# Kernel tuning notes

Hardware: AMD Instinct MI355X
Metric: run time of the kernel (lower is better)

Reference implementation:

```python
import jax, jax.numpy as jnp
import numpy as np

N_NODES = 100000


def _sage_layer(x, src, dst, Wl, Wr, b):
    # mean-aggregate source features at destination nodes
    msgs = x[src]                                                # [E, d_in]
    agg = jax.ops.segment_sum(msgs, dst, num_segments=N_NODES)  # [N, d_in]
    cnt = jax.ops.segment_sum(jnp.ones((src.shape[0], 1), x.dtype), dst,
                              num_segments=N_NODES)             # [N, 1]
    mean = agg / jnp.maximum(cnt, 1.0)
    # PyG SAGEConv: lin_l(aggr) + lin_r(x); lin_l carries the bias
    return mean @ Wl.T + x @ Wr.T + b


def setup_inputs() -> dict:
    key = jax.random.key(0)
    ks = jax.random.split(key, 9)
    d_in, d_h, d_out, E = 128, 128, 64, 1600000
    s = 1.0 / np.sqrt(d_in)
    inp = {
        "x": jax.random.normal(ks[0], (N_NODES, d_in), jnp.float32),
        "Wl0": jax.random.normal(ks[1], (d_h, d_in), jnp.float32) * s,
        "Wr0": jax.random.normal(ks[2], (d_h, d_in), jnp.float32) * s,
        "b0": jnp.zeros((d_h,), jnp.float32),
        "Wl1": jax.random.normal(ks[3], (d_h, d_h), jnp.float32) * s,
        "Wr1": jax.random.normal(ks[4], (d_h, d_h), jnp.float32) * s,
        "b1": jnp.zeros((d_h,), jnp.float32),
        "Wl2": jax.random.normal(ks[5], (d_out, d_h), jnp.float32) * s,
        "Wr2": jax.random.normal(ks[6], (d_out, d_h), jnp.float32) * s,
        "b2": jnp.zeros((d_out,), jnp.float32),
        "edge_index": jax.random.randint(ks[7], (2, E), 0, N_NODES, jnp.int64),
    }
    return inp


def reference(x, Wl0, Wr0, b0, Wl1, Wr1, b1, Wl2, Wr2, b2, edge_index):
    src, dst = edge_index[0], edge_index[1]
    h = jax.nn.relu(_sage_layer(x, src, dst, Wl0, Wr0, b0))  # dropout = identity (eval)
    h = jax.nn.relu(_sage_layer(h, src, dst, Wl1, Wr1, b1))
    return _sage_layer(h, src, dst, Wl2, Wr2, b2)
```

## Files before the change

### kernel.cpp

```cpp
#include <hip/hip_runtime.h>

#define D 128
typedef unsigned short u16;
typedef unsigned int u32;
typedef __attribute__((ext_vector_type(8))) short short8;
typedef __attribute__((ext_vector_type(16))) float float16;

__device__ __forceinline__ u16 f2bf(float f) {
    u32 u = __builtin_bit_cast(u32, f);
    u += 0x7FFFu + ((u >> 16) & 1u);
    return (u16)(u >> 16);
}
__device__ __forceinline__ float bf2f(u16 b) {
    return __builtin_bit_cast(float, ((u32)b) << 16);
}
__device__ __forceinline__ short8 zero8() {
    short8 z;
    #pragma unroll
    for (int i = 0; i < 8; ++i) z[i] = 0;
    return z;
}


__global__ __launch_bounds__(256) void hist_kernel(const int* __restrict__ dst,
        int* __restrict__ cnt, int* __restrict__ rank, int E) {
    int e = blockIdx.x * 256 + threadIdx.x;
    if (e < E) rank[e] = atomicAdd(&cnt[dst[e]], 1);
}

__global__ __launch_bounds__(256) void scan1_kernel(const int* __restrict__ cnt,
        int* __restrict__ rowptr, int* __restrict__ blksum, int N) {
    __shared__ int sdata[256];
    const int base = blockIdx.x * 1024 + threadIdx.x * 4;
    int v0 = 0, v1 = 0, v2 = 0, v3 = 0;
    if (base + 3 < N) {
        int4 q = *reinterpret_cast<const int4*>(cnt + base);
        v0 = q.x; v1 = q.y; v2 = q.z; v3 = q.w;
    } else {
        if (base + 0 < N) v0 = cnt[base + 0];
        if (base + 1 < N) v1 = cnt[base + 1];
        if (base + 2 < N) v2 = cnt[base + 2];
    }
    const int t = v0 + v1 + v2 + v3;
    int val = t;
    sdata[threadIdx.x] = val;
    __syncthreads();
    for (int off = 1; off < 256; off <<= 1) {
        int other = (threadIdx.x >= off) ? sdata[threadIdx.x - off] : 0;
        __syncthreads();
        val += other;
        sdata[threadIdx.x] = val;
        __syncthreads();
    }
    const int excl = val - t;
    if (base + 0 < N) rowptr[base + 0] = excl;
    if (base + 1 < N) rowptr[base + 1] = excl + v0;
    if (base + 2 < N) rowptr[base + 2] = excl + v0 + v1;
    if (base + 3 < N) rowptr[base + 3] = excl + v0 + v1 + v2;
    if (threadIdx.x == 255) blksum[blockIdx.x] = val;
}

__global__ __launch_bounds__(256) void scan2_kernel(int* __restrict__ blksum, int nb) {
    __shared__ int s[256];
    const int t = threadIdx.x;
    const int v = (t < nb) ? blksum[t] : 0;
    int val = v;
    s[t] = val;
    __syncthreads();
    for (int off = 1; off < 256; off <<= 1) {
        int o = (t >= off) ? s[t - off] : 0;
        __syncthreads();
        val += o;
        s[t] = val;
        __syncthreads();
    }
    if (t < nb) blksum[t] = val - v;
    if (t == 255) blksum[nb] = val;
}

__global__ __launch_bounds__(256) void scan3_kernel(int* __restrict__ rowptr,
        const int* __restrict__ blksum, int N) {
    const int base = blockIdx.x * 1024 + threadIdx.x * 4;
    const int off = blksum[blockIdx.x];
    #pragma unroll
    for (int k = 0; k < 4; ++k)
        if (base + k < N) rowptr[base + k] += off;
    if (base == 0 && blockIdx.x == 0) rowptr[N] = blksum[gridDim.x];
}

__global__ __launch_bounds__(256) void invdeg_kernel(const int* __restrict__ rowptr,
        float* __restrict__ invd, int N) {
    int i = blockIdx.x * 256 + threadIdx.x;
    if (i < N) {
        int deg = rowptr[i + 1] - rowptr[i];
        invd[i] = 1.0f / (float)(deg > 1 ? deg : 1);
    }
}

__global__ __launch_bounds__(256) void fill_kernel(const int* __restrict__ src,
        const int* __restrict__ dst, const int* __restrict__ rowptr,
        const int* __restrict__ rank, int* __restrict__ colidx, int E) {
    int e = blockIdx.x * 256 + threadIdx.x;
    if (e < E) {
        int d = dst[e];
        colidx[rowptr[d] + rank[e]] = src[e];
    }
}

__global__ __launch_bounds__(256) void tobf16_kernel(const float* __restrict__ in,
        u16* __restrict__ outb, int n8) {
    int i = blockIdx.x * 256 + threadIdx.x;
    if (i >= n8) return;
    float4 a = *reinterpret_cast<const float4*>(in + (size_t)i * 8);
    float4 b = *reinterpret_cast<const float4*>(in + (size_t)i * 8 + 4);
    short8 r;
    r[0] = (short)f2bf(a.x); r[1] = (short)f2bf(a.y);
    r[2] = (short)f2bf(a.z); r[3] = (short)f2bf(a.w);
    r[4] = (short)f2bf(b.x); r[5] = (short)f2bf(b.y);
    r[6] = (short)f2bf(b.z); r[7] = (short)f2bf(b.w);
    *reinterpret_cast<short8*>(outb + (size_t)i * 8) = r;
}

__global__ __launch_bounds__(256) void gather_kernel(const u16* __restrict__ xin,
        const int* __restrict__ rowptr, const int* __restrict__ colidx,
        const float* __restrict__ invd, u16* __restrict__ outA, int N) {
    const int node = blockIdx.x * 4 + (threadIdx.x >> 6);
    if (node >= N) return;
    const int lane = threadIdx.x & 63;
    const int g = lane >> 4;
    const int r = lane & 15;
    const int beg = rowptr[node];
    const int nb = rowptr[node + 1] - beg;

    float a0 = 0.f, a1 = 0.f, a2 = 0.f, a3 = 0.f;
    float a4 = 0.f, a5 = 0.f, a6 = 0.f, a7 = 0.f;

    for (int base = 0; base < nb; base += 8) {
        const bool p0 = (base + g) < nb;
        const bool p1 = (base + 4 + g) < nb;
        uint4 v0 = make_uint4(0, 0, 0, 0), v1 = v0;
        if (p0) {
            int s0 = colidx[beg + base + g];
            v0 = *reinterpret_cast<const uint4*>(xin + (size_t)s0 * D + r * 8);
        }
        if (p1) {
            int s1 = colidx[beg + base + 4 + g];
            v1 = *reinterpret_cast<const uint4*>(xin + (size_t)s1 * D + r * 8);
        }
        a0 += bf2f((u16)v0.x) + bf2f((u16)v1.x);
        a1 += bf2f((u16)(v0.x >> 16)) + bf2f((u16)(v1.x >> 16));
        a2 += bf2f((u16)v0.y) + bf2f((u16)v1.y);
        a3 += bf2f((u16)(v0.y >> 16)) + bf2f((u16)(v1.y >> 16));
        a4 += bf2f((u16)v0.z) + bf2f((u16)v1.z);
        a5 += bf2f((u16)(v0.z >> 16)) + bf2f((u16)(v1.z >> 16));
        a6 += bf2f((u16)v0.w) + bf2f((u16)v1.w);
        a7 += bf2f((u16)(v0.w >> 16)) + bf2f((u16)(v1.w >> 16));
    }

    #pragma unroll
    for (int m = 16; m <= 32; m <<= 1) {
        a0 += __shfl_xor(a0, m, 64); a1 += __shfl_xor(a1, m, 64);
        a2 += __shfl_xor(a2, m, 64); a3 += __shfl_xor(a3, m, 64);
        a4 += __shfl_xor(a4, m, 64); a5 += __shfl_xor(a5, m, 64);
        a6 += __shfl_xor(a6, m, 64); a7 += __shfl_xor(a7, m, 64);
    }

    if (g == 0) {
        const float ic = invd[node];
        uint4 o;
        o.x = (u32)f2bf(a0 * ic) | ((u32)f2bf(a1 * ic) << 16);
        o.y = (u32)f2bf(a2 * ic) | ((u32)f2bf(a3 * ic) << 16);
        o.z = (u32)f2bf(a4 * ic) | ((u32)f2bf(a5 * ic) << 16);
        o.w = (u32)f2bf(a6 * ic) | ((u32)f2bf(a7 * ic) << 16);
        *reinterpret_cast<uint4*>(outA + (size_t)node * D + r * 8) = o;
    }
}

__global__ __launch_bounds__(256) void gather64_kernel(const u16* __restrict__ yin,
        const int* __restrict__ rowptr, const int* __restrict__ colidx,
        const float* __restrict__ invd, u16* __restrict__ outM, int N) {
    const int node = blockIdx.x * 4 + (threadIdx.x >> 6);
    if (node >= N) return;
    const int lane = threadIdx.x & 63;
    const int g = lane >> 4;
    const int r = lane & 15;
    const int beg = rowptr[node];
    const int nb = rowptr[node + 1] - beg;

    float a0 = 0.f, a1 = 0.f, a2 = 0.f, a3 = 0.f;

    for (int base = 0; base < nb; base += 8) {
        const bool p0 = (base + g) < nb;
        const bool p1 = (base + 4 + g) < nb;
        uint2 v0 = make_uint2(0, 0), v1 = v0;
        if (p0) {
            int s0 = colidx[beg + base + g];
            v0 = *reinterpret_cast<const uint2*>(yin + (size_t)s0 * 64 + r * 4);
        }
        if (p1) {
            int s1 = colidx[beg + base + 4 + g];
            v1 = *reinterpret_cast<const uint2*>(yin + (size_t)s1 * 64 + r * 4);
        }
        a0 += bf2f((u16)v0.x) + bf2f((u16)v1.x);
        a1 += bf2f((u16)(v0.x >> 16)) + bf2f((u16)(v1.x >> 16));
        a2 += bf2f((u16)v0.y) + bf2f((u16)v1.y);
        a3 += bf2f((u16)(v0.y >> 16)) + bf2f((u16)(v1.y >> 16));
    }

    #pragma unroll
    for (int m = 16; m <= 32; m <<= 1) {
        a0 += __shfl_xor(a0, m, 64); a1 += __shfl_xor(a1, m, 64);
        a2 += __shfl_xor(a2, m, 64); a3 += __shfl_xor(a3, m, 64);
    }

    if (g == 0) {
        const float ic = invd[node];
        uint2 o;
        o.x = (u32)f2bf(a0 * ic) | ((u32)f2bf(a1 * ic) << 16);
        o.y = (u32)f2bf(a2 * ic) | ((u32)f2bf(a3 * ic) << 16);
        *reinterpret_cast<uint2*>(outM + (size_t)node * 64 + r * 4) = o;
    }
}

template<int DOUT, bool RELU, bool BF16OUT>
__global__ __launch_bounds__(256) void sage_gemm(
    const u16* __restrict__ Abf, const u16* __restrict__ Xbf,
    const float* __restrict__ Wl, const float* __restrict__ Wr,
    const float* __restrict__ bias, float* __restrict__ outf,
    u16* __restrict__ outb, int N, int nchunks)
{
    constexpr int BM = 256;
    constexpr int NKB = 4;
    constexpr int WR = (DOUT == 128) ? 2 : 4;
    constexpr int WC = 4 / WR;
    constexpr int WTM = BM / WR;
    constexpr int WTN = DOUT / WC;
    constexpr int MR = WTM / 32;
    constexpr int NC = WTN / 32;
    constexpr int LDA = 72;
    constexpr int LDW = 264;

    __shared__ u16 sW[DOUT][LDW];
    __shared__ u16 sA[2][BM][LDA];

    const int tid = threadIdx.x;
    const int lane = tid & 63;
    const int w = tid >> 6;
    const int wr = w % WR;
    const int wc = w / WR;

    for (int i = tid; i < DOUT * 64; i += 256) {
        const int c = i >> 6, q = i & 63;
        const float* sp = (q < 32) ? (Wl + (size_t)c * 128 + q * 4)
                                   : (Wr + (size_t)c * 128 + (q - 32) * 4);
        float4 wv = *reinterpret_cast<const float4*>(sp);
        u32* dp = reinterpret_cast<u32*>(&sW[c][q * 4]);
        dp[0] = (u32)f2bf(wv.x) | ((u32)f2bf(wv.y) << 16);
        dp[1] = (u32)f2bf(wv.z) | ((u32)f2bf(wv.w) << 16);
    }

    short8 rg[2][4];

    auto STAGE = [&](int kb, int m0) {
        const u16* srcb = (kb < 2) ? Abf : Xbf;
        const int koff = (kb & 1) * 64;
        #pragma unroll
        for (int p = 0; p < 2; ++p) {
            const int r = (tid >> 1) + p * 128;
            const int row = m0 + r;
            const u16* sp = srcb + (size_t)row * D + koff + (tid & 1) * 32;
            if (row < N) {
                #pragma unroll
                for (int uu = 0; uu < 4; ++uu)
                    rg[p][uu] = *reinterpret_cast<const short8*>(sp + uu * 8);
            } else {
                #pragma unroll
                for (int uu = 0; uu < 4; ++uu) rg[p][uu] = zero8();
            }
        }
    };
    auto WLDS = [&](int buf) {
        #pragma unroll
        for (int p = 0; p < 2; ++p) {
            const int r = (tid >> 1) + p * 128;
            u16* dp = &sA[buf][r][(tid & 1) * 32];
            #pragma unroll
            for (int uu = 0; uu < 4; ++uu)
                *reinterpret_cast<short8*>(dp + uu * 8) = rg[p][uu];
        }
    };

    for (int chunk = blockIdx.x; chunk < nchunks; chunk += gridDim.x) {
        const int m0 = chunk * BM;
        STAGE(0, m0);
        __syncthreads();
        WLDS(0);

        float16 acc[MR][NC];
        #pragma unroll
        for (int mi = 0; mi < MR; ++mi)
            #pragma unroll
            for (int ni = 0; ni < NC; ++ni)
                #pragma unroll
                for (int e = 0; e < 16; ++e) acc[mi][ni][e] = 0.f;

        #pragma unroll
        for (int kb = 0; kb < NKB; ++kb) {
            if (kb + 1 < NKB) STAGE(kb + 1, m0);
            __syncthreads();
            #pragma unroll
            for (int ks = 0; ks < 4; ++ks) {
                short8 af[MR], bfv[NC];
                #pragma unroll
                for (int mi = 0; mi < MR; ++mi)
                    af[mi] = *reinterpret_cast<const short8*>(
                        &sA[kb & 1][wr * WTM + mi * 32 + (lane & 31)]
                           [ks * 16 + (lane >> 5) * 8]);
                #pragma unroll
                for (int ni = 0; ni < NC; ++ni)
                    bfv[ni] = *reinterpret_cast<const short8*>(
                        &sW[wc * WTN + ni * 32 + (lane & 31)]
                           [kb * 64 + ks * 16 + (lane >> 5) * 8]);
                #pragma unroll
                for (int mi = 0; mi < MR; ++mi)
                    #pragma unroll
                    for (int ni = 0; ni < NC; ++ni)
                        acc[mi][ni] = __builtin_amdgcn_mfma_f32_32x32x16_bf16(
                            af[mi], bfv[ni], acc[mi][ni], 0, 0, 0);
            }
            if (kb + 1 < NKB) WLDS((kb + 1) & 1);
        }

        #pragma unroll
        for (int ni = 0; ni < NC; ++ni) {
            const int col = wc * WTN + ni * 32 + (lane & 31);
            const float bv = bias[col];
            #pragma unroll
            for (int mi = 0; mi < MR; ++mi) {
                #pragma unroll
                for (int e = 0; e < 16; ++e) {
                    const int row = wr * WTM + mi * 32 + 4 * (lane >> 5)
                                    + (e & 3) + 8 * (e >> 2);
                    const int grow = m0 + row;
                    if (grow < N) {
                        float v = acc[mi][ni][e] + bv;
                        if (RELU) v = fmaxf(v, 0.f);
                        if (BF16OUT) outb[(size_t)grow * DOUT + col] = f2bf(v);
                        else         outf[(size_t)grow * DOUT + col] = v;
                    }
                }
            }
        }
    }
}

template<bool ADDMEAN, bool BF16OUT, bool BIAS>
__global__ __launch_bounds__(256) void lin_gemm(
    const u16* __restrict__ In, const float* __restrict__ W,
    const float* __restrict__ bias, const u16* __restrict__ mean2,
    float* __restrict__ outf, u16* __restrict__ outb, int N, int nchunks)
{
    constexpr int DOUT = 64;
    constexpr int BM = 256;
    constexpr int NKB = 2;
    constexpr int WTM = 64;
    constexpr int MR = 2, NC = 2;
    constexpr int LDA = 72;
    constexpr int LDW = 136;

    __shared__ u16 sW[DOUT][LDW];
    __shared__ u16 sA[2][BM][LDA];

    const int tid = threadIdx.x;
    const int lane = tid & 63;
    const int wr = tid >> 6;

    for (int i = tid; i < DOUT * 32; i += 256) {
        const int c = i >> 5, q = i & 31;
        float4 wv = *reinterpret_cast<const float4*>(W + (size_t)c * 128 + q * 4);
        u32* dp = reinterpret_cast<u32*>(&sW[c][q * 4]);
        dp[0] = (u32)f2bf(wv.x) | ((u32)f2bf(wv.y) << 16);
        dp[1] = (u32)f2bf(wv.z) | ((u32)f2bf(wv.w) << 16);
    }

    short8 rg[2][4];

    auto STAGE = [&](int kb, int m0) {
        const int koff = kb * 64;
        #pragma unroll
        for (int p = 0; p < 2; ++p) {
            const int r = (tid >> 1) + p * 128;
            const int row = m0 + r;
            const u16* sp = In + (size_t)row * D + koff + (tid & 1) * 32;
            if (row < N) {
                #pragma unroll
                for (int uu = 0; uu < 4; ++uu)
                    rg[p][uu] = *reinterpret_cast<const short8*>(sp + uu * 8);
            } else {
                #pragma unroll
                for (int uu = 0; uu < 4; ++uu) rg[p][uu] = zero8();
            }
        }
    };
    auto WLDS = [&](int buf) {
        #pragma unroll
        for (int p = 0; p < 2; ++p) {
            const int r = (tid >> 1) + p * 128;
            u16* dp = &sA[buf][r][(tid & 1) * 32];
            #pragma unroll
            for (int uu = 0; uu < 4; ++uu)
                *reinterpret_cast<short8*>(dp + uu * 8) = rg[p][uu];
        }
    };

    for (int chunk = blockIdx.x; chunk < nchunks; chunk += gridDim.x) {
        const int m0 = chunk * BM;
        STAGE(0, m0);
        __syncthreads();
        WLDS(0);

        float16 acc[MR][NC];
        #pragma unroll
        for (int mi = 0; mi < MR; ++mi)
            #pragma unroll
            for (int ni = 0; ni < NC; ++ni)
                #pragma unroll
                for (int e = 0; e < 16; ++e) acc[mi][ni][e] = 0.f;

        #pragma unroll
        for (int kb = 0; kb < NKB; ++kb) {
            if (kb + 1 < NKB) STAGE(kb + 1, m0);
            __syncthreads();
            #pragma unroll
            for (int ks = 0; ks < 4; ++ks) {
                short8 af[MR], bfv[NC];
                #pragma unroll
                for (int mi = 0; mi < MR; ++mi)
                    af[mi] = *reinterpret_cast<const short8*>(
                        &sA[kb & 1][wr * WTM + mi * 32 + (lane & 31)]
                           [ks * 16 + (lane >> 5) * 8]);
                #pragma unroll
                for (int ni = 0; ni < NC; ++ni)
                    bfv[ni] = *reinterpret_cast<const short8*>(
                        &sW[ni * 32 + (lane & 31)]
                           [kb * 64 + ks * 16 + (lane >> 5) * 8]);
                #pragma unroll
                for (int mi = 0; mi < MR; ++mi)
                    #pragma unroll
                    for (int ni = 0; ni < NC; ++ni)
                        acc[mi][ni] = __builtin_amdgcn_mfma_f32_32x32x16_bf16(
                            af[mi], bfv[ni], acc[mi][ni], 0, 0, 0);
            }
            if (kb + 1 < NKB) WLDS((kb + 1) & 1);
        }

        #pragma unroll
        for (int ni = 0; ni < NC; ++ni) {
            const int col = ni * 32 + (lane & 31);
            const float bv = BIAS ? bias[col] : 0.f;
            #pragma unroll
            for (int mi = 0; mi < MR; ++mi) {
                #pragma unroll
                for (int e = 0; e < 16; ++e) {
                    const int row = wr * WTM + mi * 32 + 4 * (lane >> 5)
                                    + (e & 3) + 8 * (e >> 2);
                    const int grow = m0 + row;
                    if (grow < N) {
                        float v = acc[mi][ni][e] + bv;
                        if (ADDMEAN) v += bf2f(mean2[(size_t)grow * 64 + col]);
                        if (BF16OUT) outb[(size_t)grow * DOUT + col] = f2bf(v);
                        else         outf[(size_t)grow * DOUT + col] = v;
                    }
                }
            }
        }
    }
}

extern "C" void kernel_launch(void* const* d_in, const int* in_sizes, int n_in,
                              void* d_out, int out_size, void* d_ws, size_t ws_size,
                              hipStream_t stream) {
    const float* x   = (const float*)d_in[0];
    const float* Wl0 = (const float*)d_in[1];
    const float* Wr0 = (const float*)d_in[2];
    const float* b0  = (const float*)d_in[3];
    const float* Wl1 = (const float*)d_in[4];
    const float* Wr1 = (const float*)d_in[5];
    const float* b1  = (const float*)d_in[6];
    const float* Wl2 = (const float*)d_in[7];
    const float* Wr2 = (const float*)d_in[8];
    const float* b2  = (const float*)d_in[9];
    const int* ei    = (const int*)d_in[10];

    const int E = in_sizes[10] / 2;
    const int N = in_sizes[0] / D;
    const int* src = ei;
    const int* dst = ei + E;

    u16* Xbf = (u16*)d_ws;
    u16* Abf = Xbf + (size_t)N * D;
    u16* H0  = Abf + (size_t)N * D;
    u16* H1  = H0 + (size_t)N * D;
    float* invd   = (float*)(H1 + (size_t)N * D);
    int*   cnt    = (int*)(invd + N);
    int*   rowptr = cnt + N;
    int*   blksum = rowptr + N + 8;
    int*   colidx = blksum + 512;
    int*   rank   = colidx + E;
    float* out = (float*)d_out;

    u16* y2    = Abf;
    u16* mean2 = Abf + (size_t)N * 64;

    const int NB = (N + 1023) / 1024;

    hipMemsetAsync(cnt, 0, (size_t)N * sizeof(int), stream);
    hist_kernel <<<(E + 255) / 256, 256, 0, stream>>>(dst, cnt, rank, E);
    scan1_kernel<<<NB, 256, 0, stream>>>(cnt, rowptr, blksum, N);
    scan2_kernel<<<1, 256, 0, stream>>>(blksum, NB);
    scan3_kernel<<<NB, 256, 0, stream>>>(rowptr, blksum, N);
    invdeg_kernel<<<(N + 255) / 256, 256, 0, stream>>>(rowptr, invd, N);
    fill_kernel <<<(E + 255) / 256, 256, 0, stream>>>(src, dst, rowptr, rank, colidx, E);

    tobf16_kernel<<<(N * D / 8 + 255) / 256, 256, 0, stream>>>(x, Xbf, N * D / 8);

    const int ggrid = (N + 3) / 4;
    const int nchunks = (N + 255) / 256;
    const int ggemm = (nchunks + 1) / 2;

    gather_kernel<<<ggrid, 256, 0, stream>>>(Xbf, rowptr, colidx, invd, Abf, N);
    sage_gemm<128, true, true><<<ggemm, 256, 0, stream>>>(
        Abf, Xbf, Wl0, Wr0, b0, nullptr, H0, N, nchunks);

    gather_kernel<<<ggrid, 256, 0, stream>>>(H0, rowptr, colidx, invd, Abf, N);
    sage_gemm<128, true, true><<<ggemm, 256, 0, stream>>>(
        Abf, H0, Wl1, Wr1, b1, nullptr, H1, N, nchunks);

    lin_gemm<false, true, false><<<ggemm, 256, 0, stream>>>(
        H1, Wl2, nullptr, nullptr, nullptr, y2, N, nchunks);
    gather64_kernel<<<ggrid, 256, 0, stream>>>(y2, rowptr, colidx, invd, mean2, N);
    lin_gemm<true, false, true><<<ggemm, 256, 0, stream>>>(
        H1, Wr2, b2, mean2, out, nullptr, N, nchunks);
}
```

Baseline: 518.7 us.

## Shard degree histogram atomics and fuse bf16 cast into histogram kernel

```diff
diff --git a/kernel.cpp b/kernel.cpp
--- a/kernel.cpp
+++ b/kernel.cpp
@@ -1,6 +1,7 @@
 #include <hip/hip_runtime.h>
 
 #define D 128
+#define NSHARD 8
 typedef unsigned short u16;
 typedef unsigned int u32;
 typedef __attribute__((ext_vector_type(8))) short short8;
@@ -22,10 +23,45 @@
 }
 
 
-__global__ __launch_bounds__(256) void hist_kernel(const int* __restrict__ dst,
-        int* __restrict__ cnt, int* __restrict__ rank, int E) {
-    int e = blockIdx.x * 256 + threadIdx.x;
-    if (e < E) rank[e] = atomicAdd(&cnt[dst[e]], 1);
+__global__ __launch_bounds__(256) void hist_tobf16_kernel(
+        const int* __restrict__ dst, int* __restrict__ cntS,
+        int* __restrict__ rank, int E, int N, int nblkA,
+        const float* __restrict__ xin, u16* __restrict__ xb, int n8) {
+    if ((int)blockIdx.x < nblkA) {
+        const int e = blockIdx.x * 256 + threadIdx.x;
+        if (e < E) {
+            const int shard = blockIdx.x & (NSHARD - 1);
+            rank[e] = atomicAdd(&cntS[(size_t)shard * N + dst[e]], 1);
+        }
+    } else {
+        const int i = (blockIdx.x - nblkA) * 256 + threadIdx.x;
+        if (i < n8) {
+            float4 a = *reinterpret_cast<const float4*>(xin + (size_t)i * 8);
+            float4 b = *reinterpret_cast<const float4*>(xin + (size_t)i * 8 + 4);
+            short8 r;
+            r[0] = (short)f2bf(a.x); r[1] = (short)f2bf(a.y);
+            r[2] = (short)f2bf(a.z); r[3] = (short)f2bf(a.w);
+            r[4] = (short)f2bf(b.x); r[5] = (short)f2bf(b.y);
+            r[6] = (short)f2bf(b.z); r[7] = (short)f2bf(b.w);
+            *reinterpret_cast<short8*>(xb + (size_t)i * 8) = r;
+        }
+    }
+}
+
+__global__ __launch_bounds__(256) void shardoff_kernel(
+        const int* __restrict__ cntS, int* __restrict__ off,
+        int* __restrict__ cnttot, float* __restrict__ invd, int N) {
+    const int d = blockIdx.x * 256 + threadIdx.x;
+    if (d >= N) return;
+    int run = 0;
+    #pragma unroll
+    for (int s = 0; s < NSHARD; ++s) {
+        const int c = cntS[(size_t)s * N + d];
+        off[(size_t)s * N + d] = run;
+        run += c;
+    }
+    cnttot[d] = run;
+    invd[d] = 1.0f / (float)(run > 1 ? run : 1);
 }
 
 __global__ __launch_bounds__(256) void scan1_kernel(const int* __restrict__ cnt,
@@ -88,37 +124,16 @@
     if (base == 0 && blockIdx.x == 0) rowptr[N] = blksum[gridDim.x];
 }
 
-__global__ __launch_bounds__(256) void invdeg_kernel(const int* __restrict__ rowptr,
-        float* __restrict__ invd, int N) {
-    int i = blockIdx.x * 256 + threadIdx.x;
-    if (i < N) {
-        int deg = rowptr[i + 1] - rowptr[i];
-        invd[i] = 1.0f / (float)(deg > 1 ? deg : 1);
-    }
-}
-
 __global__ __launch_bounds__(256) void fill_kernel(const int* __restrict__ src,
         const int* __restrict__ dst, const int* __restrict__ rowptr,
-        const int* __restrict__ rank, int* __restrict__ colidx, int E) {
-    int e = blockIdx.x * 256 + threadIdx.x;
+        const int* __restrict__ off, const int* __restrict__ rank,
+        int* __restrict__ colidx, int E, int N) {
+    const int e = blockIdx.x * 256 + threadIdx.x;
     if (e < E) {
-        int d = dst[e];
-        colidx[rowptr[d] + rank[e]] = src[e];
-    }
-}
-
-__global__ __launch_bounds__(256) void tobf16_kernel(const float* __restrict__ in,
-        u16* __restrict__ outb, int n8) {
-    int i = blockIdx.x * 256 + threadIdx.x;
-    if (i >= n8) return;
-    float4 a = *reinterpret_cast<const float4*>(in + (size_t)i * 8);
-    float4 b = *reinterpret_cast<const float4*>(in + (size_t)i * 8 + 4);
-    short8 r;
-    r[0] = (short)f2bf(a.x); r[1] = (short)f2bf(a.y);
-    r[2] = (short)f2bf(a.z); r[3] = (short)f2bf(a.w);
-    r[4] = (short)f2bf(b.x); r[5] = (short)f2bf(b.y);
-    r[6] = (short)f2bf(b.z); r[7] = (short)f2bf(b.w);
-    *reinterpret_cast<short8*>(outb + (size_t)i * 8) = r;
+        const int d = dst[e];
+        const int shard = (e >> 8) & (NSHARD - 1);
+        colidx[rowptr[d] + off[(size_t)shard * N + d] + rank[e]] = src[e];
+    }
 }
 
 __global__ __launch_bounds__(256) void gather_kernel(const u16* __restrict__ xin,
@@ -502,8 +517,10 @@
     u16* H0  = Abf + (size_t)N * D;
     u16* H1  = H0 + (size_t)N * D;
     float* invd   = (float*)(H1 + (size_t)N * D);
-    int*   cnt    = (int*)(invd + N);
-    int*   rowptr = cnt + N;
+    int*   cntS   = (int*)(invd + N);
+    int*   off    = cntS + (size_t)NSHARD * N;
+    int*   cnttot = off + (size_t)NSHARD * N;
+    int*   rowptr = cnttot + N;
     int*   blksum = rowptr + N + 8;
     int*   colidx = blksum + 512;
     int*   rank   = colidx + E;
@@ -513,16 +530,18 @@
     u16* mean2 = Abf + (size_t)N * 64;
 
     const int NB = (N + 1023) / 1024;
-
-    hipMemsetAsync(cnt, 0, (size_t)N * sizeof(int), stream);
-    hist_kernel <<<(E + 255) / 256, 256, 0, stream>>>(dst, cnt, rank, E);
-    scan1_kernel<<<NB, 256, 0, stream>>>(cnt, rowptr, blksum, N);
+    const int nblkA = (E + 255) / 256;
+    const int n8 = N * D / 8;
+    const int nblkB = (n8 + 255) / 256;
+
+    hipMemsetAsync(cntS, 0, (size_t)NSHARD * N * sizeof(int), stream);
+    hist_tobf16_kernel<<<nblkA + nblkB, 256, 0, stream>>>(
+        dst, cntS, rank, E, N, nblkA, x, Xbf, n8);
+    shardoff_kernel<<<(N + 255) / 256, 256, 0, stream>>>(cntS, off, cnttot, invd, N);
+    scan1_kernel<<<NB, 256, 0, stream>>>(cnttot, rowptr, blksum, N);
     scan2_kernel<<<1, 256, 0, stream>>>(blksum, NB);
     scan3_kernel<<<NB, 256, 0, stream>>>(rowptr, blksum, N);
-    invdeg_kernel<<<(N + 255) / 256, 256, 0, stream>>>(rowptr, invd, N);
-    fill_kernel <<<(E + 255) / 256, 256, 0, stream>>>(src, dst, rowptr, rank, colidx, E);
-
-    tobf16_kernel<<<(N * D / 8 + 255) / 256, 256, 0, stream>>>(x, Xbf, N * D / 8);
+    fill_kernel <<<nblkA, 256, 0, stream>>>(src, dst, rowptr, off, rank, colidx, E, N);
 
     const int ggrid = (N + 3) / 4;
     const int nchunks = (N + 255) / 256;
```

Measured after the change: 523.8 us. Within noise of the previous version (+1.0%).
